# Kernel tuning notes

Measured on AMD Instinct MI355X. Metric: run time of the kernel, lower is better.

Reference implementation:

```python
import jax, jax.numpy as jnp
import numpy as np

N_GROUPS = 8
TOPK_GROUPS = 4
TOP_K = 8
SCALING_FACTOR = 2.5
NORM_WEIGHTS = True


def setup_inputs() -> dict:
    key = jax.random.key(0)
    k1, k2 = jax.random.split(key)
    T, D, E = 32768, 2048, 256
    hidden_tensor = jax.random.normal(k1, (T, D), dtype=jnp.float32)
    weight = jax.random.normal(k2, (E, D), dtype=jnp.float32) * (1.0 / np.sqrt(D))
    scores_bias = jnp.full((E,), 0.001, dtype=jnp.float32)
    return {"hidden_tensor": hidden_tensor, "weight": weight, "scores_bias": scores_bias}


def reference(hidden_tensor, weight, scores_bias):
    T = hidden_tensor.shape[0]
    E = weight.shape[0]
    gsize = E // N_GROUPS
    # router logits -> sigmoid gate scores  [T, E]
    scores = jax.nn.sigmoid(hidden_tensor.astype(jnp.float32) @ weight.astype(jnp.float32).T)
    # group masking is done under no_grad in the original module
    s = jax.lax.stop_gradient(scores) + scores_bias[None, :]
    sg = s.reshape(T, N_GROUPS, gsize)                       # [T, G, E/G]
    top2_vals, _ = jax.lax.top_k(sg, 2)                      # [T, G, 2]
    group_scores = top2_vals.sum(-1)                         # [T, G]
    _, top_groups = jax.lax.top_k(group_scores, TOPK_GROUPS)  # [T, KG]
    group_mask = jnp.zeros((T, N_GROUPS), dtype=bool)
    group_mask = group_mask.at[jnp.arange(T)[:, None], top_groups].set(True)
    masked = jnp.where(group_mask[:, :, None], sg, 0.0).reshape(T, E)
    # top-k experts within the allowed groups
    _, expert_idx = jax.lax.top_k(masked, TOP_K)             # [T, K]
    # gather original (un-biased) sigmoid scores for the selected experts
    weights = jnp.take_along_axis(scores, expert_idx, axis=1)  # [T, K]
    if NORM_WEIGHTS:
        weights = weights / weights.sum(-1, keepdims=True)
    weights = weights * SCALING_FACTOR
    return expert_idx, weights
```

## Files before the change

kernel.cpp:

```cpp
#include <hip/hip_runtime.h>
#include <math.h>

#define T_TOKENS 32768
#define DIM      2048
#define NEXP     256
#define NGROUP   8
#define GSIZE    32
#define TOPG     4
#define TOPK     8
#define SCALE    2.5
#define TAU      1e-5f

#define BM  64
#define NIT 32
#define SC_STRIDE 257

#define RLIST_OFF 16
#define WPACK_OFF_BYTES (1 << 18)

typedef __attribute__((ext_vector_type(8))) short bf16x8;
typedef __attribute__((ext_vector_type(8))) unsigned short u16x8;
typedef __attribute__((ext_vector_type(4))) float f32x4;

__device__ __forceinline__ unsigned short f2bf_rne(float f) {
    unsigned u = __float_as_uint(f);
    u += 0x7fffu + ((u >> 16) & 1u);
    return (unsigned short)(u >> 16);
}
__device__ __forceinline__ float bf2f(unsigned short h) {
    return __uint_as_float(((unsigned)h) << 16);
}

__device__ __forceinline__ void lds_barrier() {
    __builtin_amdgcn_sched_barrier(0);
    asm volatile("s_waitcnt lgkmcnt(0)" ::: "memory");
    __builtin_amdgcn_s_barrier();
    __builtin_amdgcn_sched_barrier(0);
}

__global__ void pack_w_kernel(const float* __restrict__ Wt,
                              unsigned short* __restrict__ wp,
                              int* __restrict__ ws) {
    if (blockIdx.x == 0 && threadIdx.x == 0) ws[0] = 0;
    const int slot = blockIdx.x * 256 + threadIdx.x;
    const int lane = slot & 63;
    const int n    = (slot >> 6) & 15;
    const int s    = slot >> 10;
    const int e    = n * 16 + (lane & 15);
    const int k0   = s * 32 + (lane >> 4) * 8;
    const float* src = Wt + (size_t)e * DIM + k0;
    const float4 v0 = *(const float4*)src;
    const float4 v1 = *(const float4*)(src + 4);
    const float a[8] = {v0.x, v0.y, v0.z, v0.w, v1.x, v1.y, v1.z, v1.w};
    union { unsigned short u[8]; u16x8 v; } uh, ul;
    #pragma unroll
    for (int i = 0; i < 8; ++i) {
        const unsigned short hb = f2bf_rne(a[i]);
        uh.u[i] = hb;
        ul.u[i] = f2bf_rne(a[i] - bf2f(hb));
    }
    const size_t base = ((size_t)(s * 16 + n) * 2) * 64 + lane;
    *(u16x8*)(wp + base * 8)        = uh.v;
    *(u16x8*)(wp + (base + 64) * 8) = ul.v;
}

__global__ __launch_bounds__(512, 4) void router_main(
    const float* __restrict__ H,
    const float* __restrict__ bias,
    const unsigned short* __restrict__ wp,
    float* __restrict__ out,
    int* __restrict__ ws)
{
    __shared__ __align__(16) char smraw[BM * SC_STRIDE * 4];
    __shared__ float biasS[NEXP];

    typedef unsigned short AhlBuf[2][2][4][64][8];
    AhlBuf* Ahl = reinterpret_cast<AhlBuf*>(smraw);
    float*  Sc  = reinterpret_cast<float*>(smraw);

    const int tid  = threadIdx.x;
    const int lane = tid & 63;
    const int w    = tid >> 6;
    const int t0   = blockIdx.x * BM;

    if (tid < NEXP) biasS[tid] = bias[tid];

    f32x4 acc[4][2];
    #pragma unroll
    for (int m = 0; m < 4; ++m)
        #pragma unroll
        for (int jj = 0; jj < 2; ++jj)
            acc[m][jj] = (f32x4){0.f, 0.f, 0.f, 0.f};

    const int arow = tid >> 3;
    const int koct = tid & 7;
    const int sub  = koct >> 2;
    const int kq   = koct & 3;
    const int am   = arow >> 4;
    const int lw   = (kq << 4) | (((arow & 15) ^ (kq << 1) ^ sub) & 15);
    const float* Aptr = H + (size_t)(t0 + arow) * DIM + koct * 8;

    auto loadH = [&](int it, float4& x0, float4& x1) {
        const float* p = Aptr + (size_t)it * 64;
        x0 = *(const float4*)p;
        x1 = *(const float4*)(p + 4);
    };
    auto stageIter = [&](int b, const float4& x0, const float4& x1) {
        const float a[8] = {x0.x, x0.y, x0.z, x0.w, x1.x, x1.y, x1.z, x1.w};
        union { unsigned short u[8]; u16x8 v; } uh, ul;
        #pragma unroll
        for (int i = 0; i < 8; ++i) {
            const unsigned short hb = f2bf_rne(a[i]);
            uh.u[i] = hb;
            ul.u[i] = f2bf_rne(a[i] - bf2f(hb));
        }
        *(u16x8*)&Ahl[b][sub][0][am][lw][0] = uh.v;
        *(u16x8*)&Ahl[b][sub][1][am][lw][0] = ul.v;
    };
    auto loadB = [&](int s, bf16x8 (&Bh)[2], bf16x8 (&Bl)[2]) {
        #pragma unroll
        for (int jj = 0; jj < 2; ++jj) {
            const size_t slot = ((size_t)(s * 16 + 2 * w + jj) * 2) * 64 + lane;
            Bh[jj] = *(const bf16x8*)(wp + slot * 8);
            Bl[jj] = *(const bf16x8*)(wp + (slot + 64) * 8);
        }
    };
    auto computeSub = [&](int b, int ss, bf16x8 (&Bh)[2], bf16x8 (&Bl)[2]) {
        const int rslot = (lane & 48) | (((lane & 15) ^ ((lane >> 4) << 1) ^ ss) & 15);
        bf16x8 Ah[4], Al[4];
        #pragma unroll
        for (int m = 0; m < 4; ++m) {
            Ah[m] = *(const bf16x8*)&Ahl[b][ss][0][m][rslot][0];
            Al[m] = *(const bf16x8*)&Ahl[b][ss][1][m][rslot][0];
        }
        __builtin_amdgcn_s_setprio(1);
        #pragma unroll
        for (int m = 0; m < 4; ++m)
            #pragma unroll
            for (int jj = 0; jj < 2; ++jj) {
                acc[m][jj] = __builtin_amdgcn_mfma_f32_16x16x32_bf16(Al[m], Bh[jj], acc[m][jj], 0, 0, 0);
                acc[m][jj] = __builtin_amdgcn_mfma_f32_16x16x32_bf16(Ah[m], Bl[jj], acc[m][jj], 0, 0, 0);
                acc[m][jj] = __builtin_amdgcn_mfma_f32_16x16x32_bf16(Ah[m], Bh[jj], acc[m][jj], 0, 0, 0);
            }
        __builtin_amdgcn_s_setprio(0);
    };

    bf16x8 Ba_h[2], Ba_l[2], Bb_h[2], Bb_l[2];
    float4 hS0, hS1, hL0, hL1;

    {
        float4 c0, c1;
        loadH(0, c0, c1);
        stageIter(0, c0, c1);
    }
    loadH(1, hS0, hS1);
    loadB(0, Ba_h, Ba_l);
    lds_barrier();

    for (int it = 0; it < NIT; it += 2) {
        loadH(min(it + 2, NIT - 1), hL0, hL1);
        stageIter(1, hS0, hS1);
        loadB(2 * it + 1, Bb_h, Bb_l);
        computeSub(0, 0, Ba_h, Ba_l);
        loadB(min(2 * it + 2, 2 * NIT - 1), Ba_h, Ba_l);
        computeSub(0, 1, Bb_h, Bb_l);
        lds_barrier();

        loadH(min(it + 3, NIT - 1), hS0, hS1);
        if (it + 2 < NIT) stageIter(0, hL0, hL1);
        loadB(min(2 * it + 3, 2 * NIT - 1), Bb_h, Bb_l);
        computeSub(1, 0, Ba_h, Ba_l);
        loadB(min(2 * it + 4, 2 * NIT - 1), Ba_h, Ba_l);
        computeSub(1, 1, Bb_h, Bb_l);
        lds_barrier();
    }

    const int rbase = (lane >> 4) * 4;
    const int cc    = lane & 15;
    #pragma unroll
    for (int m = 0; m < 4; ++m)
        #pragma unroll
        for (int jj = 0; jj < 2; ++jj)
            #pragma unroll
            for (int r = 0; r < 4; ++r) {
                const int token  = 16 * m + rbase + r;
                const int expert = 16 * (2 * w + jj) + cc;
                const float sg = 1.0f / (1.0f + expf(-acc[m][jj][r]));
                Sc[token * SC_STRIDE + expert] = sg + biasS[expert];
            }
    __syncthreads();

    if (tid < BM) {
        float* row = &Sc[tid * SC_STRIDE];

        float gs[NGROUP];
        for (int g = 0; g < NGROUP; ++g) {
            const int base = g * GSIZE;
            float m1 = -3e38f, m2 = -3e38f;
            for (int j = 0; j < GSIZE; ++j) {
                const float v = row[base + j];
                if (v > m1) { m2 = m1; m1 = v; }
                else if (v > m2) { m2 = v; }
            }
            gs[g] = m1 + m2;
        }

        unsigned gsel = 0;
        float minSel = 3e38f, maxUn = -3e38f;
        #pragma unroll
        for (int g = 0; g < NGROUP; ++g) {
            int rank = 0;
            #pragma unroll
            for (int h = 0; h < NGROUP; ++h)
                rank += (gs[h] > gs[g]) || (gs[h] == gs[g] && h < g);
            if (rank < TOPG) { gsel |= 1u << g; minSel = fminf(minSel, gs[g]); }
            else             { maxUn = fmaxf(maxUn, gs[g]); }
        }
        float minMargin = minSel - maxUn;

        float wk[TOPK];
        int   ik[TOPK];
        float wsum = 0.0f;
        float prev = 3e38f;
        #pragma unroll
        for (int k = 0; k < TOPK + 1; ++k) {
            float bv = -3e38f;
            int   bi = 0;
            for (int g = 0; g < NGROUP; ++g) {
                if (!((gsel >> g) & 1u)) continue;
                const int base = g * GSIZE;
                for (int j = 0; j < GSIZE; ++j) {
                    const int e = base + j;
                    const float v = row[e];
                    if (v > bv) { bv = v; bi = e; }
                }
            }
            if (k > 0) minMargin = fminf(minMargin, prev - bv);
            prev = bv;
            if (k < TOPK) {
                const float wv = bv - biasS[bi];
                wk[k] = wv; ik[k] = bi; wsum += wv;
                row[bi] = -3e38f;
            }
        }

        const float norm = (float)SCALE / wsum;
        const size_t t = (size_t)(t0 + tid);
        float* oi = out + t * TOPK;
        float* ow = out + (size_t)T_TOKENS * TOPK + t * TOPK;
        #pragma unroll
        for (int k = 0; k < TOPK; ++k) {
            oi[k] = (float)ik[k];
            ow[k] = wk[k] * norm;
        }

        if (minMargin < TAU) {
            const int r = atomicAdd(ws, 1);
            ws[RLIST_OFF + r] = t0 + tid;
        }
    }
}

__global__ __launch_bounds__(512) void router_rescue(
    const float* __restrict__ H,
    const float* __restrict__ Wt,
    const float* __restrict__ bias,
    float* __restrict__ out,
    const int* __restrict__ ws)
{
    __shared__ float  Hrow[DIM];
    __shared__ double PartD[2][NEXP];
    __shared__ double Sd[NEXP];
    __shared__ double biasD[NEXP];

    const int tid = threadIdx.x;
    const int nR  = ws[0];
    const int re  = tid & 255;
    const int kh  = tid >> 8;

    if (tid < NEXP) biasD[tid] = (double)bias[tid];

    for (int idx = blockIdx.x; idx < nR; idx += gridDim.x) {
        const size_t t = (size_t)ws[RLIST_OFF + idx];
        __syncthreads();

        *(float4*)&Hrow[tid * 4] = *(const float4*)&H[t * DIM + tid * 4];
        __syncthreads();

        {
            const float* wr = Wt + (size_t)re * DIM + kh * 1024;
            const float* hr = Hrow + kh * 1024;
            double c0 = 0.0, c1 = 0.0, c2 = 0.0, c3 = 0.0;
            #pragma unroll 4
            for (int k = 0; k < 1024; k += 4) {
                const float4 wv = *(const float4*)(wr + k);
                c0 = fma((double)hr[k + 0], (double)wv.x, c0);
                c1 = fma((double)hr[k + 1], (double)wv.y, c1);
                c2 = fma((double)hr[k + 2], (double)wv.z, c2);
                c3 = fma((double)hr[k + 3], (double)wv.w, c3);
            }
            PartD[kh][re] = ((c0 + c1) + c2) + c3;
        }
        __syncthreads();

        if (tid < NEXP) {
            const double sum = PartD[0][tid] + PartD[1][tid];
            Sd[tid] = 1.0 / (1.0 + exp(-sum)) + biasD[tid];
        }
        __syncthreads();

        if (tid < 64) {
            const int lane = tid;
            const int e0   = lane * 4;
            const int gm   = lane >> 3;

            double sv[4];
            #pragma unroll
            for (int j = 0; j < 4; ++j) sv[j] = Sd[e0 + j];

            double m1 = sv[0], m2 = -1e300;
            #pragma unroll
            for (int j = 1; j < 4; ++j) {
                if (sv[j] > m1) { m2 = m1; m1 = sv[j]; }
                else if (sv[j] > m2) { m2 = sv[j]; }
            }
            #pragma unroll
            for (int mask = 1; mask <= 4; mask <<= 1) {
                const double o1 = __shfl_xor(m1, mask);
                const double o2 = __shfl_xor(m2, mask);
                const double lo = fmin(m1, o1);
                m1 = fmax(m1, o1);
                m2 = fmax(lo, fmax(m2, o2));
            }
            const double gsm = m1 + m2;

            double gsd[NGROUP];
            #pragma unroll
            for (int g = 0; g < NGROUP; ++g) gsd[g] = __shfl(gsm, g * 8);

            unsigned gsel = 0;
            #pragma unroll
            for (int g = 0; g < NGROUP; ++g) {
                int rank = 0;
                #pragma unroll
                for (int h = 0; h < NGROUP; ++h)
                    rank += (gsd[h] > gsd[g]) || (gsd[h] == gsd[g] && h < g);
                if (rank < TOPG) gsel |= 1u << g;
            }
            const bool allowed = (gsel >> gm) & 1u;

            double wkd[TOPK];
            int    ikd[TOPK];
            double wsum = 0.0;
            #pragma unroll
            for (int k = 0; k < TOPK; ++k) {
                double bv = -1e300;
                int    be = 1 << 30;
                if (allowed) {
                    #pragma unroll
                    for (int j = 0; j < 4; ++j)
                        if (sv[j] > bv) { bv = sv[j]; be = e0 + j; }
                }
                #pragma unroll
                for (int mask = 1; mask <= 32; mask <<= 1) {
                    const double ov = __shfl_xor(bv, mask);
                    const int    oe = __shfl_xor(be, mask);
                    if (ov > bv || (ov == bv && oe < be)) { bv = ov; be = oe; }
                }
                const double wv = bv - biasD[be];
                wkd[k] = wv; ikd[k] = be; wsum += wv;
                const bool own = ((be >> 2) == lane);
                #pragma unroll
                for (int j = 0; j < 4; ++j)
                    if (own && (be & 3) == j) sv[j] = -1e300;
            }

            if (lane == 0) {
                const double norm = SCALE / wsum;
                float* oi = out + t * TOPK;
                float* ow = out + (size_t)T_TOKENS * TOPK + t * TOPK;
                #pragma unroll
                for (int k = 0; k < TOPK; ++k) {
                    oi[k] = (float)ikd[k];
                    ow[k] = (float)(wkd[k] * norm);
                }
            }
        }
    }
}

extern "C" void kernel_launch(void* const* d_in, const int* in_sizes, int n_in,
                              void* d_out, int out_size, void* d_ws, size_t ws_size,
                              hipStream_t stream) {
    const float* H    = (const float*)d_in[0];
    const float* Wt   = (const float*)d_in[1];
    const float* bias = (const float*)d_in[2];
    float* out = (float*)d_out;
    int*   ws  = (int*)d_ws;
    unsigned short* wp = (unsigned short*)((char*)d_ws + WPACK_OFF_BYTES);

    pack_w_kernel<<<256, 256, 0, stream>>>(Wt, wp, ws);
    router_main<<<T_TOKENS / BM, 512, 0, stream>>>(H, bias, wp, out, ws);
    router_rescue<<<1024, 512, 0, stream>>>(H, Wt, bias, out, ws);
}
```

Before: 203.2 us.

## Batch four rescue tokens per block to reuse weight loads

The fp64 rescue kernel now handles four flagged tokens per block iteration. Each weight float4 is loaded once and applied to all four hidden rows held in shared memory, which cuts redundant weight traffic. The final top-k selection runs on one wave per token, and the grid shrinks from 1024 to 256 blocks. This raises shared memory and register use per block, and when nt is below four the unused Hs rows are still read as stale data, though their results are never used.

```diff
diff --git a/kernel.cpp b/kernel.cpp
--- a/kernel.cpp
+++ b/kernel.cpp
@@ -261,6 +261,7 @@
     }
 }
 
+#define RB 4
 __global__ __launch_bounds__(512) void router_rescue(
     const float* __restrict__ H,
     const float* __restrict__ Wt,
@@ -268,55 +269,79 @@
     float* __restrict__ out,
     const int* __restrict__ ws)
 {
-    __shared__ float  Hrow[DIM];
-    __shared__ double PartD[2][NEXP];
-    __shared__ double Sd[NEXP];
+    __shared__ float  Hs[RB][DIM];
+    __shared__ double PartD[2][RB][NEXP];
+    __shared__ double Sd[RB][NEXP];
     __shared__ double biasD[NEXP];
 
-    const int tid = threadIdx.x;
-    const int nR  = ws[0];
-    const int re  = tid & 255;
-    const int kh  = tid >> 8;
+    const int tid  = threadIdx.x;
+    const int lane = tid & 63;
+    const int wv_  = tid >> 6;
+    const int nR   = ws[0];
+    const int re   = tid & 255;
+    const int kh   = tid >> 8;
 
     if (tid < NEXP) biasD[tid] = (double)bias[tid];
 
-    for (int idx = blockIdx.x; idx < nR; idx += gridDim.x) {
-        const size_t t = (size_t)ws[RLIST_OFF + idx];
+    for (int base = blockIdx.x * RB; base < nR; base += gridDim.x * RB) {
+        const int nt = min(RB, nR - base);
         __syncthreads();
 
-        *(float4*)&Hrow[tid * 4] = *(const float4*)&H[t * DIM + tid * 4];
+        for (int j = 0; j < nt; ++j) {
+            const size_t t = (size_t)ws[RLIST_OFF + base + j];
+            *(float4*)&Hs[j][tid * 4] = *(const float4*)&H[t * DIM + tid * 4];
+        }
         __syncthreads();
 
         {
             const float* wr = Wt + (size_t)re * DIM + kh * 1024;
-            const float* hr = Hrow + kh * 1024;
-            double c0 = 0.0, c1 = 0.0, c2 = 0.0, c3 = 0.0;
-            #pragma unroll 4
+            const float* h0 = &Hs[0][kh * 1024];
+            const float* h1 = &Hs[1][kh * 1024];
+            const float* h2 = &Hs[2][kh * 1024];
+            const float* h3 = &Hs[3][kh * 1024];
+            double a0 = 0.0, a1 = 0.0, a2 = 0.0, a3 = 0.0;
+            #pragma unroll 2
             for (int k = 0; k < 1024; k += 4) {
-                const float4 wv = *(const float4*)(wr + k);
-                c0 = fma((double)hr[k + 0], (double)wv.x, c0);
-                c1 = fma((double)hr[k + 1], (double)wv.y, c1);
-                c2 = fma((double)hr[k + 2], (double)wv.z, c2);
-                c3 = fma((double)hr[k + 3], (double)wv.w, c3);
-            }
-            PartD[kh][re] = ((c0 + c1) + c2) + c3;
+                const float4 wf = *(const float4*)(wr + k);
+                const double w0 = (double)wf.x, w1 = (double)wf.y;
+                const double w2 = (double)wf.z, w3 = (double)wf.w;
+                const float4 x0 = *(const float4*)(h0 + k);
+                const float4 x1 = *(const float4*)(h1 + k);
+                const float4 x2 = *(const float4*)(h2 + k);
+                const float4 x3 = *(const float4*)(h3 + k);
+                a0 = fma((double)x0.x, w0, a0); a1 = fma((double)x1.x, w0, a1);
+                a2 = fma((double)x2.x, w0, a2); a3 = fma((double)x3.x, w0, a3);
+                a0 = fma((double)x0.y, w1, a0); a1 = fma((double)x1.y, w1, a1);
+                a2 = fma((double)x2.y, w1, a2); a3 = fma((double)x3.y, w1, a3);
+                a0 = fma((double)x0.z, w2, a0); a1 = fma((double)x1.z, w2, a1);
+                a2 = fma((double)x2.z, w2, a2); a3 = fma((double)x3.z, w2, a3);
+                a0 = fma((double)x0.w, w3, a0); a1 = fma((double)x1.w, w3, a1);
+                a2 = fma((double)x2.w, w3, a2); a3 = fma((double)x3.w, w3, a3);
+            }
+            PartD[kh][0][re] = a0;
+            PartD[kh][1][re] = a1;
+            PartD[kh][2][re] = a2;
+            PartD[kh][3][re] = a3;
         }
         __syncthreads();
 
         if (tid < NEXP) {
-            const double sum = PartD[0][tid] + PartD[1][tid];
-            Sd[tid] = 1.0 / (1.0 + exp(-sum)) + biasD[tid];
+            #pragma unroll
+            for (int j = 0; j < RB; ++j) {
+                const double sum = PartD[0][j][tid] + PartD[1][j][tid];
+                Sd[j][tid] = 1.0 / (1.0 + exp(-sum)) + biasD[tid];
+            }
         }
         __syncthreads();
 
-        if (tid < 64) {
-            const int lane = tid;
-            const int e0   = lane * 4;
-            const int gm   = lane >> 3;
+        if (wv_ < nt) {
+            const int e0 = lane * 4;
+            const int gm = lane >> 3;
+            const size_t t = (size_t)ws[RLIST_OFF + base + wv_];
 
             double sv[4];
             #pragma unroll
-            for (int j = 0; j < 4; ++j) sv[j] = Sd[e0 + j];
+            for (int j = 0; j < 4; ++j) sv[j] = Sd[wv_][e0 + j];
 
             double m1 = sv[0], m2 = -1e300;
             #pragma unroll
@@ -367,8 +392,8 @@
                     const int    oe = __shfl_xor(be, mask);
                     if (ov > bv || (ov == bv && oe < be)) { bv = ov; be = oe; }
                 }
-                const double wv = bv - biasD[be];
-                wkd[k] = wv; ikd[k] = be; wsum += wv;
+                const double wvv = bv - biasD[be];
+                wkd[k] = wvv; ikd[k] = be; wsum += wvv;
                 const bool own = ((be >> 2) == lane);
                 #pragma unroll
                 for (int j = 0; j < 4; ++j)
@@ -401,5 +426,5 @@
 
     pack_w_kernel<<<256, 256, 0, stream>>>(Wt, wp, ws);
     router_main<<<T_TOKENS / BM, 512, 0, stream>>>(H, bias, wp, out, ws);
-    router_rescue<<<1024, 512, 0, stream>>>(H, Wt, bias, out, ws);
-}
+    router_rescue<<<256, 512, 0, stream>>>(H, Wt, bias, out, ws);
+}
```

Result: slower. 210.5 us (+3.6%).
